# Optimization experiments

Hardware: AMD Instinct MI355X
Metric: run time of the kernel (lower is better)

The kernel has to match this reference:

```python
import jax, jax.numpy as jnp
import numpy as np

B, T, E = 2, 2048, 1024
H = 16
D = E // H  # head_dim = 64


def setup_inputs() -> dict:
    key = jax.random.key(0)
    k1, k2, k3 = jax.random.split(key, 3)
    x = jax.random.normal(k1, (B, T, E), dtype=jnp.float32)
    w_qkv = jax.random.normal(k2, (3 * E, E), dtype=jnp.float32) * 0.02
    w_proj = jax.random.normal(k3, (E, E), dtype=jnp.float32) * 0.02
    return {"x": x, "w_qkv": w_qkv, "w_proj": w_proj}


def reference(x, w_qkv, w_proj):
    b, t, c = x.shape
    # qkv projection (torch Linear: x @ W^T), split into q,k,v
    qkv = jnp.einsum('btc,fc->btf', x, w_qkv)  # [B,T,3E]
    q, k, v = jnp.split(qkv, 3, axis=-1)
    # [B,T,E] -> [B,H,T,D]
    q = q.reshape(b, t, H, D).transpose(0, 2, 1, 3)
    k = k.reshape(b, t, H, D).transpose(0, 2, 1, 3)
    v = v.reshape(b, t, H, D).transpose(0, 2, 1, 3)
    scale = 1.0 / jnp.sqrt(jnp.float32(D))
    att = jnp.einsum('bhqd,bhkd->bhqk', q, k) * scale  # [B,H,T,T]
    causal = jnp.tril(jnp.ones((t, t), dtype=bool))
    att = jnp.where(causal[None, None], att, -jnp.inf)
    att = jax.nn.softmax(att, axis=-1)
    out = jnp.einsum('bhqk,bhkd->bhqd', att, v)  # [B,H,T,D]
    out = out.transpose(0, 2, 1, 3).reshape(b, t, c)  # [B,T,E]
    out = jnp.einsum('btc,oc->bto', out, w_proj)
    return out
```

## Files before the change

kernel.cpp:

```cpp
#include <hip/hip_runtime.h>
#include <stdint.h>
#include <stddef.h>

typedef __attribute__((ext_vector_type(8))) short s16x8;
typedef __attribute__((ext_vector_type(4))) short s16x4;
typedef __attribute__((ext_vector_type(4))) float f32x4;

#define B_  2
#define T_  2048
#define E_  1024
#define H_  16
#define E3_ 3072

__device__ __forceinline__ short f2bf(float f) {
  union { float f; uint32_t u; } v; v.f = f;
  uint32_t u = v.u;
  return (short)((u + 0x7FFFu + ((u >> 16) & 1u)) >> 16);
}

__device__ __forceinline__ void gload_lds16(const short* g, short* l) {
  __builtin_amdgcn_global_load_lds(
      (__attribute__((address_space(1))) void*)(const_cast<short*>(g)),
      (__attribute__((address_space(3))) void*)(l), 16, 0, 0);
}

__global__ void castk_all(const float* __restrict__ x, const float* __restrict__ wqkv,
                          const float* __restrict__ wproj, short* __restrict__ xb,
                          short* __restrict__ wqkvb, short* __restrict__ wprojb) {
  const int bid = blockIdx.x;
  const float* in; short* out; int i; float sc = 1.0f;
  if (bid < 4096)      { in = x;     out = xb;     i = bid * 256 + threadIdx.x; }
  else if (bid < 7168) { in = wqkv;  out = wqkvb;  i = (bid - 4096) * 256 + threadIdx.x;
                         if (i < 262144) sc = 0.18033688011112042f; }
  else                 { in = wproj; out = wprojb; i = (bid - 7168) * 256 + threadIdx.x; }
  const float4 v = ((const float4*)in)[i];
  s16x4 o;
  o[0] = f2bf(v.x * sc); o[1] = f2bf(v.y * sc);
  o[2] = f2bf(v.z * sc); o[3] = f2bf(v.w * sc);
  ((s16x4*)out)[i] = o;
}

template <int MODE>
__global__ void gemm_nt_128(const short* __restrict__ A, const short* __restrict__ B,
                            void* __restrict__ Cv, short* __restrict__ vt,
                            int M, int N, int K) {
  __shared__ short As[128 * 32];
  __shared__ short Bs[128 * 32];
  const int tid  = threadIdx.x;
  const int lane = tid & 63;
  const int w    = tid >> 6;
  const int quad = lane >> 4;
  const int l16  = lane & 15;
  const int wm   = (w >> 1) * 64;
  const int wn   = (w & 1) * 64;
  const int bm   = blockIdx.y * 128;
  const int bn   = blockIdx.x * 128;

  f32x4 acc[4][4];
#pragma unroll
  for (int i = 0; i < 4; i++)
#pragma unroll
    for (int j = 0; j < 4; j++) acc[i][j] = (f32x4){0.f, 0.f, 0.f, 0.f};

  const int srow = w * 32 + (lane >> 2);
  const int scol = (lane & 3) * 8;
  const short* gA = A + (size_t)(bm + srow) * K + scol;
  const short* gB = B + (size_t)(bn + srow) * K + scol;
  short* lA = As + (w * 32) * 32;
  short* lB = Bs + (w * 32) * 32;

  for (int k0 = 0; k0 < K; k0 += 32) {
    __syncthreads();
    gload_lds16(gA + k0,          lA);
    gload_lds16(gA + 16 * K + k0, lA + 16 * 32);
    gload_lds16(gB + k0,          lB);
    gload_lds16(gB + 16 * K + k0, lB + 16 * 32);
    __syncthreads();

    s16x8 a[4], b[4];
#pragma unroll
    for (int i = 0; i < 4; i++)
      a[i] = *(const s16x8*)&As[(wm + i * 16 + l16) * 32 + quad * 8];
#pragma unroll
    for (int j = 0; j < 4; j++)
      b[j] = *(const s16x8*)&Bs[(wn + j * 16 + l16) * 32 + quad * 8];
#pragma unroll
    for (int i = 0; i < 4; i++)
#pragma unroll
      for (int j = 0; j < 4; j++)
        acc[i][j] = __builtin_amdgcn_mfma_f32_16x16x32_bf16(a[i], b[j], acc[i][j], 0, 0, 0);
  }

  if (MODE == 2 && bn >= 2 * E_) {
#pragma unroll
    for (int i = 0; i < 4; i++) {
      const int token = bm + wm + i * 16 + quad * 4;
      const int bb = token >> 11, t = token & (T_ - 1);
#pragma unroll
      for (int j = 0; j < 4; j++) {
        const int col = bn + wn + j * 16 + l16 - 2 * E_;
        s16x4 pk;
#pragma unroll
        for (int r = 0; r < 4; r++) pk[r] = f2bf(acc[i][j][r]);
        *(s16x4*)&vt[((size_t)(bb * H_ + (col >> 6)) * 64 + (col & 63)) * T_ + t] = pk;
      }
    }
  } else {
#pragma unroll
    for (int i = 0; i < 4; i++) {
      const int row0 = bm + wm + i * 16 + quad * 4;
#pragma unroll
      for (int j = 0; j < 4; j++) {
        const int col = bn + wn + j * 16 + l16;
#pragma unroll
        for (int r = 0; r < 4; r++) {
          const size_t idx = (size_t)(row0 + r) * N + col;
          if (MODE == 2) ((short*)Cv)[idx] = f2bf(acc[i][j][r]);
          else           ((float*)Cv)[idx] = acc[i][j][r];
        }
      }
    }
  }
}

__global__ void __launch_bounds__(256, 4)
attn_kernel(const short* __restrict__ qkv, const short* __restrict__ vt,
            short* __restrict__ attout) {
  __shared__ short Ks[2][64 * 64];
  __shared__ short Vs[2][64 * 64];
  const int tid  = threadIdx.x;
  const int lane = tid & 63;
  const int w    = tid >> 6;
  const int quad = lane >> 4;
  const int l16  = lane & 15;
  const int bh = blockIdx.x;
  const int b = bh >> 4, h = bh & 15;
  const int ya = blockIdx.y & 7, yb = blockIdx.y >> 3;
  const int qt = (3 - yb) * 8 + ((yb & 1) ? ya : (7 - ya));
  const int q0b = qt * 64;
  const int q0w = q0b + w * 16;
  const float NEG_INF = -__builtin_inff();

  const int srl = lane >> 3;
  const int sgc = ((lane & 7) ^ srl) * 8;
  const short* gK = qkv + (size_t)(b * T_) * E3_ + E_ + h * 64 + sgc;
  const short* gV = vt + (size_t)(bh * 64) * T_ + sgc;
  const int swz = (l16 & 7);

  s16x8 ones;
#pragma unroll
  for (int i = 0; i < 8; i++) ones[i] = (short)0x3F80;

  auto stage = [&](int kv0s, int bf) {
#pragma unroll
    for (int i = 0; i < 2; i++) {
      const int r8 = w * 16 + i * 8;
      const int rowp = r8 + srl;
      const int rowk = (rowp & ~12) | ((rowp & 4) << 1) | ((rowp & 8) >> 1);
      gload_lds16(gK + (size_t)(kv0s + rowk) * E3_, &Ks[bf][r8 * 64]);
      gload_lds16(gV + (size_t)rowp * T_ + kv0s,    &Vs[bf][r8 * 64]);
    }
  };

  const short* qbase = qkv + (size_t)(b * T_ + q0w + l16) * E3_ + h * 64 + quad * 8;
  const s16x8 qf0 = *(const s16x8*)(qbase);
  const s16x8 qf1 = *(const s16x8*)(qbase + 32);

  f32x4 o[4]; f32x4 ol = (f32x4){0.f, 0.f, 0.f, 0.f};
#pragma unroll
  for (int j = 0; j < 4; j++) o[j] = (f32x4){0.f, 0.f, 0.f, 0.f};

  stage(0, 0);
  __syncthreads();

  for (int kv0 = 0, g = 0; kv0 <= q0b; kv0 += 64, g++) {
    const int cur = g & 1;

    s16x8 kf[2][4];
#pragma unroll
    for (int c = 0; c < 2; c++)
#pragma unroll
      for (int j = 0; j < 4; j++)
        kf[c][j] = *(const s16x8*)&Ks[cur][(j * 16 + l16) * 64 + (((c * 4 + quad) ^ swz) * 8)];

    if (kv0 + 64 <= q0b) stage(kv0 + 64, cur ^ 1);

    f32x4 s[4];
#pragma unroll
    for (int j = 0; j < 4; j++) s[j] = (f32x4){0.f, 0.f, 0.f, 0.f};
    __builtin_amdgcn_s_setprio(1);
#pragma unroll
    for (int c = 0; c < 2; c++)
#pragma unroll
      for (int j = 0; j < 4; j++)
        s[j] = __builtin_amdgcn_mfma_f32_16x16x32_bf16(kf[c][j], c == 0 ? qf0 : qf1, s[j], 0, 0, 0);
    __builtin_amdgcn_s_setprio(0);

    if (kv0 == q0b) {
      const int tq4 = ((quad & 1) << 3) | ((quad >> 1) << 2);
#pragma unroll
      for (int j = 0; j < 4; j++)
#pragma unroll
        for (int r = 0; r < 4; r++)
          if (j * 16 + tq4 + r > w * 16 + l16) s[j][r] = NEG_INF;
    }

#pragma unroll
    for (int j = 0; j < 4; j++) {
      s[j][0] = __builtin_amdgcn_exp2f(s[j][0]);
      s[j][1] = __builtin_amdgcn_exp2f(s[j][1]);
      s[j][2] = __builtin_amdgcn_exp2f(s[j][2]);
      s[j][3] = __builtin_amdgcn_exp2f(s[j][3]);
    }

    int dj[4][2];
#pragma unroll
    for (int j = 0; j < 4; j++) {
      asm("v_cvt_pk_bf16_f32 %0, %1, %2" : "=v"(dj[j][0]) : "v"(s[j][0]), "v"(s[j][1]));
      asm("v_cvt_pk_bf16_f32 %0, %1, %2" : "=v"(dj[j][1]) : "v"(s[j][2]), "v"(s[j][3]));
    }

    s16x8 F[2];
#pragma unroll
    for (int c = 0; c < 2; c++) {
      int x0 = dj[2 * c][0], y0 = dj[2 * c + 1][0];
      int x1 = dj[2 * c][1], y1 = dj[2 * c + 1][1];
      asm("v_permlane32_swap_b32 %0, %1" : "+v"(x0), "+v"(y0));
      asm("v_permlane32_swap_b32 %0, %1" : "+v"(x1), "+v"(y1));
      union { int i4[4]; s16x8 v; } u;
      u.i4[0] = x0; u.i4[1] = x1; u.i4[2] = y0; u.i4[3] = y1;
      F[c] = u.v;
    }

    __builtin_amdgcn_s_setprio(1);
#pragma unroll
    for (int c = 0; c < 2; c++) {
      ol = __builtin_amdgcn_mfma_f32_16x16x32_bf16(ones, F[c], ol, 0, 0, 0);
#pragma unroll
      for (int j = 0; j < 4; j++) {
        const s16x8 vf = *(const s16x8*)&Vs[cur][(j * 16 + l16) * 64 + (((c * 4 + quad) ^ swz) * 8)];
        o[j] = __builtin_amdgcn_mfma_f32_16x16x32_bf16(vf, F[c], o[j], 0, 0, 0);
      }
    }
    __builtin_amdgcn_s_setprio(0);

    __syncthreads();
  }

  const float inv = 1.0f / ol[0];
  const int q = q0w + l16;
  short* ob = attout + ((size_t)(b * T_ + q) * H_ + h) * 64 + quad * 4;
#pragma unroll
  for (int j = 0; j < 4; j++) {
    s16x4 pk;
#pragma unroll
    for (int r = 0; r < 4; r++) pk[r] = f2bf(o[j][r] * inv);
    *(s16x4*)&ob[16 * j] = pk;
  }
}

extern "C" void kernel_launch(void* const* d_in, const int* in_sizes, int n_in,
                              void* d_out, int out_size, void* d_ws, size_t ws_size,
                              hipStream_t stream) {
  const float* x     = (const float*)d_in[0];
  const float* wqkv  = (const float*)d_in[1];
  const float* wproj = (const float*)d_in[2];

  if (ws_size < 58720256u) return;
  short* ws     = (short*)d_ws;
  short* xb     = ws;
  short* wqkvb  = xb + 4194304;
  short* wprojb = wqkvb + 3145728;
  short* qkv    = wprojb + 1048576;
  short* vt     = qkv + 12582912;
  short* attb   = vt + 4194304;

  castk_all<<<8192, 256, 0, stream>>>(x, wqkv, wproj, xb, wqkvb, wprojb);
  gemm_nt_128<2><<<dim3(24, 32), 256, 0, stream>>>(xb, wqkvb, qkv, vt, 4096, 3072, 1024);
  attn_kernel<<<dim3(32, 32), 256, 0, stream>>>(qkv, vt, attb);
  gemm_nt_128<0><<<dim3(8, 32), 256, 0, stream>>>(attb, wprojb, d_out, nullptr, 4096, 1024, 1024);
}
```

Before: 163.2 us.

## Replace QKV GEMM with 256x256-tile double-buffered swizzled LDS kernel

Adds a dedicated QKV projection GEMM that uses 256x256 output tiles with 512 threads, a K-step of 64, double-buffered LDS loaded via global_load_lds, and an XOR swizzle to avoid LDS bank conflicts. The next tile's loads are interleaved with MFMA work, and s_setprio raises priority around the MFMA bursts. The generic 128-tile GEMM drops its V-transpose path, and only the output projection still uses it. Larger tiles raise data reuse per global load, but the QKV launch shrinks to 192 blocks (fewer than the CU count) and uses 128 KB of LDS per block, which may limit occupancy.

```diff
diff --git a/kernel.cpp b/kernel.cpp
--- a/kernel.cpp
+++ b/kernel.cpp
@@ -91,9 +91,125 @@
         acc[i][j] = __builtin_amdgcn_mfma_f32_16x16x32_bf16(a[i], b[j], acc[i][j], 0, 0, 0);
   }
 
-  if (MODE == 2 && bn >= 2 * E_) {
-#pragma unroll
-    for (int i = 0; i < 4; i++) {
+#pragma unroll
+  for (int i = 0; i < 4; i++) {
+    const int row0 = bm + wm + i * 16 + quad * 4;
+#pragma unroll
+    for (int j = 0; j < 4; j++) {
+      const int col = bn + wn + j * 16 + l16;
+#pragma unroll
+      for (int r = 0; r < 4; r++) {
+        const size_t idx = (size_t)(row0 + r) * N + col;
+        if (MODE == 2) ((short*)Cv)[idx] = f2bf(acc[i][j][r]);
+        else           ((float*)Cv)[idx] = acc[i][j][r];
+      }
+    }
+  }
+}
+
+__global__ void __launch_bounds__(512, 2)
+gemm256_qkv(const short* __restrict__ A, const short* __restrict__ B,
+            short* __restrict__ qkv, short* __restrict__ vt) {
+  __shared__ short As[2][256 * 64];
+  __shared__ short Bs[2][256 * 64];
+  const int tid  = threadIdx.x;
+  const int lane = tid & 63;
+  const int w    = tid >> 6;
+  const int quad = lane >> 4;
+  const int l16  = lane & 15;
+  const int wm   = (w >> 2) * 128;
+  const int wn   = (w & 3) * 64;
+  const int bm   = blockIdx.y * 256;
+  const int bn   = blockIdx.x * 256;
+  const int srl  = lane >> 3;
+  const int sgc  = ((lane & 7) ^ srl) * 8;
+  const int swz  = l16 & 7;
+  const int K    = 1024;
+
+  const short* gA = A + (size_t)bm * K + sgc;
+  const short* gB = B + (size_t)bn * K + sgc;
+
+  f32x4 acc[8][4];
+#pragma unroll
+  for (int i = 0; i < 8; i++)
+#pragma unroll
+    for (int j = 0; j < 4; j++) acc[i][j] = (f32x4){0.f, 0.f, 0.f, 0.f};
+
+  auto stageA = [&](int kt1, int bfb, int i0) {
+#pragma unroll
+    for (int i = i0; i < i0 + 2; i++) {
+      const int r8 = w * 32 + i * 8;
+      gload_lds16(gA + (size_t)(r8 + srl) * K + kt1 * 64, &As[bfb][r8 * 64]);
+    }
+  };
+  auto stageB = [&](int kt1, int bfb, int i0) {
+#pragma unroll
+    for (int i = i0; i < i0 + 2; i++) {
+      const int r8 = w * 32 + i * 8;
+      gload_lds16(gB + (size_t)(r8 + srl) * K + kt1 * 64, &Bs[bfb][r8 * 64]);
+    }
+  };
+
+  stageA(0, 0, 0); stageA(0, 0, 2);
+  stageB(0, 0, 0); stageB(0, 0, 2);
+  __asm volatile("s_waitcnt vmcnt(0)" ::: "memory");
+  __builtin_amdgcn_s_barrier();
+
+#pragma unroll 1
+  for (int kt = 0; kt < 16; kt++) {
+    const int c = kt & 1;
+    const bool pre = (kt + 1 < 16);
+    const short* Ac = &As[c][0];
+    const short* Bc = &Bs[c][0];
+
+    s16x8 bf_[4][2];
+#pragma unroll
+    for (int q = 0; q < 4; q++) {
+      if (pre) {
+        if (q == 0)      stageA(kt + 1, c ^ 1, 0);
+        else if (q == 1) stageA(kt + 1, c ^ 1, 2);
+        else if (q == 2) stageB(kt + 1, c ^ 1, 0);
+        else             stageB(kt + 1, c ^ 1, 2);
+      }
+      if (q == 0) {
+#pragma unroll
+        for (int ni = 0; ni < 4; ni++)
+#pragma unroll
+          for (int kk = 0; kk < 2; kk++)
+            bf_[ni][kk] = *(const s16x8*)&Bc[(wn + ni * 16 + l16) * 64 + (((kk * 4 + quad) ^ swz) * 8)];
+      }
+      s16x8 af[2][2];
+#pragma unroll
+      for (int m2 = 0; m2 < 2; m2++)
+#pragma unroll
+        for (int kk = 0; kk < 2; kk++)
+          af[m2][kk] = *(const s16x8*)&Ac[(wm + (2 * q + m2) * 16 + l16) * 64 + (((kk * 4 + quad) ^ swz) * 8)];
+
+      __builtin_amdgcn_s_setprio(1);
+#pragma unroll
+      for (int kk = 0; kk < 2; kk++)
+#pragma unroll
+        for (int m2 = 0; m2 < 2; m2++)
+#pragma unroll
+          for (int ni = 0; ni < 4; ni++)
+            acc[2 * q + m2][ni] = __builtin_amdgcn_mfma_f32_16x16x32_bf16(
+                af[m2][kk], bf_[ni][kk], acc[2 * q + m2][ni], 0, 0, 0);
+      __builtin_amdgcn_s_setprio(0);
+
+      if (q == 3) {
+        if (pre) {
+          __asm volatile("s_waitcnt vmcnt(0)" ::: "memory");
+          __builtin_amdgcn_s_barrier();
+        }
+      } else {
+        __builtin_amdgcn_s_barrier();
+      }
+    }
+  }
+
+  if (bn >= 2 * E_) {
+#pragma unroll
+    for (int i = 0; i < 8; i++) {
       const int token = bm + wm + i * 16 + quad * 4;
       const int bb = token >> 11, t = token & (T_ - 1);
 #pragma unroll
@@ -107,17 +223,14 @@
     }
   } else {
 #pragma unroll
-    for (int i = 0; i < 4; i++) {
+    for (int i = 0; i < 8; i++) {
       const int row0 = bm + wm + i * 16 + quad * 4;
 #pragma unroll
       for (int j = 0; j < 4; j++) {
         const int col = bn + wn + j * 16 + l16;
 #pragma unroll
-        for (int r = 0; r < 4; r++) {
-          const size_t idx = (size_t)(row0 + r) * N + col;
-          if (MODE == 2) ((short*)Cv)[idx] = f2bf(acc[i][j][r]);
-          else           ((float*)Cv)[idx] = acc[i][j][r];
-        }
+        for (int r = 0; r < 4; r++)
+          qkv[(size_t)(row0 + r) * E3_ + col] = f2bf(acc[i][j][r]);
       }
     }
   }
@@ -276,7 +389,7 @@
   short* attb   = vt + 4194304;
 
   castk_all<<<8192, 256, 0, stream>>>(x, wqkv, wproj, xb, wqkvb, wprojb);
-  gemm_nt_128<2><<<dim3(24, 32), 256, 0, stream>>>(xb, wqkvb, qkv, vt, 4096, 3072, 1024);
+  gemm256_qkv<<<dim3(12, 16), 512, 0, stream>>>(xb, wqkvb, qkv, vt);
   attn_kernel<<<dim3(32, 32), 256, 0, stream>>>(qkv, vt, attb);
   gemm_nt_128<0><<<dim3(8, 32), 256, 0, stream>>>(attb, wprojb, d_out, nullptr, 4096, 1024, 1024);
 }
```

Result: slower. 175.4 us (+7.5%).
